# Kernel tuning notes

Measured on AMD Instinct MI355X. Metric: run time of the kernel, lower is better.

## Reference

```python
import jax, jax.numpy as jnp
import numpy as np

N = 100_000          # nodes
E = 1_600_000        # random edges (self-loops added inside gat_conv, as PyG does)
F_IN = 14
DIM = 8
HEADS = 8
NEG_SLOPE = 0.2      # PyG GATConv default negative_slope


def _gat_conv(x, edge_index, W, a_src, a_dst, bias, heads, dim, concat):
    """Faithful PyG GATConv (eval mode): self-loops, per-head linear,
    leaky-relu attention logits, segment softmax over dst, scatter-add."""
    n = x.shape[0]
    loop = jnp.arange(n)
    src = jnp.concatenate([edge_index[0], loop])   # source j
    dst = jnp.concatenate([edge_index[1], loop])   # target i (aggregation index)

    h = (x @ W).reshape(n, heads, dim)             # [N, H, D]
    alpha_src = jnp.einsum('nhd,hd->nh', h, a_src)  # [N, H]
    alpha_dst = jnp.einsum('nhd,hd->nh', h, a_dst)

    e = jax.nn.leaky_relu(alpha_src[src] + alpha_dst[dst], NEG_SLOPE)  # [E', H]
    # segment softmax over incoming edges of each dst node
    m = jax.ops.segment_max(e, dst, num_segments=n)                     # [N, H]
    ex = jnp.exp(e - m[dst])
    s = jax.ops.segment_sum(ex, dst, num_segments=n)
    alpha = ex / (s[dst] + 1e-16)                                       # [E', H]

    msg = h[src] * alpha[:, :, None]                                    # [E', H, D]
    out = jax.ops.segment_sum(msg, dst, num_segments=n)                 # [N, H, D]
    out = out.reshape(n, heads * dim) if concat else out.mean(axis=1)
    return out + bias


def setup_inputs() -> dict:
    key = jax.random.key(0)
    ks = jax.random.split(key, 10)
    x = jax.random.normal(ks[0], (N, F_IN), jnp.float32)
    edge_index = jax.random.randint(ks[1], (2, E), 0, N, dtype=jnp.int64)
    W1 = jax.random.normal(ks[2], (F_IN, HEADS * DIM), jnp.float32) * 0.3
    att_src1 = jax.random.normal(ks[3], (HEADS, DIM), jnp.float32) * 0.3
    att_dst1 = jax.random.normal(ks[4], (HEADS, DIM), jnp.float32) * 0.3
    bias1 = jnp.zeros((HEADS * DIM,), jnp.float32)
    W2 = jax.random.normal(ks[5], (HEADS * DIM, DIM), jnp.float32) * 0.15
    att_src2 = jax.random.normal(ks[6], (1, DIM), jnp.float32) * 0.3
    att_dst2 = jax.random.normal(ks[7], (1, DIM), jnp.float32) * 0.3
    bias2 = jnp.zeros((DIM,), jnp.float32)
    return {"x": x, "edge_index": edge_index,
            "W1": W1, "att_src1": att_src1, "att_dst1": att_dst1, "bias1": bias1,
            "W2": W2, "att_src2": att_src2, "att_dst2": att_dst2, "bias2": bias2}


def reference(x, edge_index, W1, att_src1, att_dst1, bias1,
              W2, att_src2, att_dst2, bias2):
    # dropout layers are identity in eval mode
    h = jax.nn.elu(_gat_conv(x, edge_index, W1, att_src1, att_dst1, bias1,
                             HEADS, DIM, concat=True))      # [N, 64]
    out = _gat_conv(h, edge_index, W2, att_src2, att_dst2, bias2,
                    1, DIM, concat=False)                   # [N, 8]
    return out
```

## Files before the change

### kernel.cpp

```cpp
#include <hip/hip_runtime.h>
#include <math.h>

#define F_IN 14
#define NSLOPE 0.2f
#define BSHIFT 7
#define BSZ 128
#define CAP 4096
#define NBMAX 1024
#define NCHUNKMAX 256
#define CHUNK 8192

typedef __attribute__((ext_vector_type(8))) unsigned short u16x8;

__device__ __forceinline__ float leaky(float v) { return v >= 0.f ? v : NSLOPE * v; }

__device__ __forceinline__ float b2f(unsigned short u) {
    union { float f; unsigned int i; } v; v.i = ((unsigned int)u) << 16; return v.f;
}
__device__ __forceinline__ unsigned short f2b(float f) {
    union { float f; unsigned int i; } v; v.f = f;
    unsigned int r = v.i + 0x7FFFu + ((v.i >> 16) & 1u);
    return (unsigned short)(r >> 16);
}

__device__ __forceinline__ int wave_incl_scan(int x) {
#pragma unroll
    for (int off = 1; off < 64; off <<= 1) {
        int v = __shfl_up(x, off, 64);
        if ((threadIdx.x & 63) >= off) x += v;
    }
    return x;
}


__global__ __launch_bounds__(1024)
void k_scatter_k1(const int* __restrict__ ei, int E,
                  int* __restrict__ stage, int* __restrict__ tab, int NB,
                  int nchunk,
                  const float* __restrict__ x,
                  const float* __restrict__ W1,
                  const float* __restrict__ a_src,
                  const float* __restrict__ a_dst,
                  unsigned short* __restrict__ h1b,
                  unsigned short* __restrict__ as1b,
                  float* __restrict__ ad1,
                  int N)
{
    __shared__ int hist[NBMAX];
    __shared__ int cur[NBMAX];
    __shared__ int srt[CHUNK];
    __shared__ int wsum[16];
    __shared__ float W[F_IN * 64];
    int t = threadIdx.x;
    if (blockIdx.x < (unsigned)nchunk) {
        int base = blockIdx.x * CHUNK;
        int end = min(base + CHUNK, E);
        int cnt = end - base;
        hist[t] = 0;
        __syncthreads();
        for (int k = base + t; k < end; k += 1024)
            atomicAdd(&hist[ei[E + k] >> BSHIFT], 1);
        __syncthreads();
        int hx = hist[t];
        int incl = wave_incl_scan(hx);
        int wid = t >> 6;
        if ((t & 63) == 63) wsum[wid] = incl;
        __syncthreads();
        int wpre = 0;
#pragma unroll
        for (int w = 0; w < 15; ++w) wpre += (w < wid) ? wsum[w] : 0;
        int exb = incl - hx + wpre;
        cur[t] = exb;
        if (t < NB) tab[(size_t)blockIdx.x * (NBMAX + 1) + t] = exb;
        if (t == 0) tab[(size_t)blockIdx.x * (NBMAX + 1) + NB] = cnt;
        __syncthreads();
        for (int k = base + t; k < end; k += 1024) {
            int j = ei[k];
            int i = ei[E + k];
            int key = i >> BSHIFT;
            int pos = atomicAdd(&cur[key], 1);
            srt[pos] = j | ((i & (BSZ - 1)) << 17);
        }
        __syncthreads();
        int cnt4 = cnt & ~3;
        for (int k = t * 4; k < cnt4; k += 4096) {
            int4 v = *(const int4*)&srt[k];
            *(int4*)&stage[base + k] = v;
        }
        if (t < (cnt & 3)) stage[base + cnt4 + t] = srt[cnt4 + t];
    } else {
        for (int idx = t; idx < F_IN * 64; idx += 1024) W[idx] = W1[idx];
        __syncthreads();
        int node = (blockIdx.x - nchunk) * 16 + (t >> 6);
        int f = t & 63;
        if (node >= N) return;
        const float* xr = x + (size_t)node * F_IN;
        float h = 0.f;
#pragma unroll
        for (int k = 0; k < F_IN; ++k) h += xr[k] * W[k * 64 + f];
        int head = f >> 3, d = f & 7;
        float vs = h * a_src[head * 8 + d];
        float vd = h * a_dst[head * 8 + d];
        vs += __shfl_xor(vs, 1, 8); vs += __shfl_xor(vs, 2, 8); vs += __shfl_xor(vs, 4, 8);
        vd += __shfl_xor(vd, 1, 8); vd += __shfl_xor(vd, 2, 8); vd += __shfl_xor(vd, 4, 8);
        if (d == 0) {
            as1b[node * 8 + head] = f2b(vs);
            ad1[node * 8 + head] = vd;
        }
        h1b[(size_t)node * 64 + f] = f2b(h);
    }
}


__global__ __launch_bounds__(256)
void pass2(const int* __restrict__ stage, const int* __restrict__ tab, int nchunk,
           int* __restrict__ rowstart, int* __restrict__ deg,
           int* __restrict__ csr, int N) {
    int b = blockIdx.x;
    int node0 = b << BSHIFT;
    int nn = min(BSZ, N - node0);
    int base = b * CAP;
    __shared__ int segstart[NCHUNKMAX];
    __shared__ int cum[NCHUNKMAX];
    __shared__ int hist[BSZ];
    __shared__ int cur[BSZ];
    __shared__ int wsum[4];
    __shared__ int wsum2[2];
    __shared__ int recs[CAP];
    int t = threadIdx.x;
    int len = 0, s = 0;
    if (t < nchunk) {
        const int* tr = tab + (size_t)t * (NBMAX + 1);
        s = tr[b];
        len = tr[b + 1] - s;
    }
    segstart[t] = s;
    if (t < BSZ) hist[t] = 0;
    int incl = wave_incl_scan(len);
    int wid = t >> 6;
    if ((t & 63) == 63) wsum[wid] = incl;
    __syncthreads();
    int wpre = 0;
#pragma unroll
    for (int w = 0; w < 3; ++w) wpre += (w < wid) ? wsum[w] : 0;
    cum[t] = incl + wpre;
    __syncthreads();
    int cnt = min(cum[NCHUNKMAX - 1], CAP);
    for (int k = t; k < cnt; k += 256) {
        int lo = 0, hi = NCHUNKMAX - 1;
        while (lo < hi) {
            int mid = (lo + hi) >> 1;
            if (cum[mid] > k) hi = mid; else lo = mid + 1;
        }
        int prev = lo ? cum[lo - 1] : 0;
        int r = stage[lo * CHUNK + segstart[lo] + (k - prev)];
        recs[k] = r;
        atomicAdd(&hist[r >> 17], 1);
    }
    __syncthreads();
    int hx = (t < BSZ) ? hist[t] : 0;
    int incl2 = wave_incl_scan(hx);
    if (t < BSZ && (t & 63) == 63) wsum2[t >> 6] = incl2;
    __syncthreads();
    if (t < nn) {
        int ex = incl2 - hx + ((t >= 64) ? wsum2[0] : 0);
        rowstart[node0 + t] = base + ex;
        deg[node0 + t] = hist[t];
        cur[t] = base + ex;
    }
    __syncthreads();
    for (int k = t; k < cnt; k += 256) {
        int r = recs[k];
        int pos = atomicAdd(&cur[r >> 17], 1);
        csr[pos] = r & 0x1FFFF;
    }
}


__global__ void k2_fused(const int* __restrict__ rowstart,
                         const int* __restrict__ deg,
                         const int* __restrict__ csr,
                         const unsigned short* __restrict__ h1b,
                         const unsigned short* __restrict__ as1b,
                         const float* __restrict__ ad1,
                         const float* __restrict__ bias1,
                         const float* __restrict__ W2,
                         const float* __restrict__ asw2,
                         const float* __restrict__ adw2,
                         float* __restrict__ h2,
                         float* __restrict__ as2,
                         float* __restrict__ ad2, int N)
{
    int t = threadIdx.x;
    int node = blockIdx.x * 32 + (t >> 3);
    int head = t & 7;
    if (node >= N) return;
    float adi = ad1[node * 8 + head];
    float asi = b2f(as1b[node * 8 + head]);
    float ex = __expf(leaky(asi + adi));
    float den = ex;
    u16x8 a = *(const u16x8*)(h1b + (size_t)node * 64 + head * 8);
    float n[8];
#pragma unroll
    for (int u = 0; u < 8; ++u) n[u] = ex * b2f(a[u]);
    int base = rowstart[node], cnt = deg[node];
    int k = 0;
    for (; k + 4 <= cnt; k += 4) {
        int j0 = csr[base + k];
        int j1 = csr[base + k + 1];
        int j2 = csr[base + k + 2];
        int j3 = csr[base + k + 3];
        float e0 = __expf(leaky(b2f(as1b[j0 * 8 + head]) + adi));
        float e1 = __expf(leaky(b2f(as1b[j1 * 8 + head]) + adi));
        float e2 = __expf(leaky(b2f(as1b[j2 * 8 + head]) + adi));
        float e3 = __expf(leaky(b2f(as1b[j3 * 8 + head]) + adi));
        u16x8 r0 = *(const u16x8*)(h1b + (size_t)j0 * 64 + head * 8);
        u16x8 r1 = *(const u16x8*)(h1b + (size_t)j1 * 64 + head * 8);
        u16x8 r2 = *(const u16x8*)(h1b + (size_t)j2 * 64 + head * 8);
        u16x8 r3 = *(const u16x8*)(h1b + (size_t)j3 * 64 + head * 8);
        den += (e0 + e1) + (e2 + e3);
#pragma unroll
        for (int u = 0; u < 8; ++u)
            n[u] += (e0 * b2f(r0[u]) + e1 * b2f(r1[u])) + (e2 * b2f(r2[u]) + e3 * b2f(r3[u]));
    }
    for (; k < cnt; ++k) {
        int j0 = csr[base + k];
        float e0 = __expf(leaky(b2f(as1b[j0 * 8 + head]) + adi));
        u16x8 r0 = *(const u16x8*)(h1b + (size_t)j0 * 64 + head * 8);
        den += e0;
#pragma unroll
        for (int u = 0; u < 8; ++u) n[u] += e0 * b2f(r0[u]);
    }
    float inv = 1.f / (den + 1e-16f);
    float v[8];
    const float* bp = bias1 + head * 8;
#pragma unroll
    for (int u = 0; u < 8; ++u) {
        float w = n[u] * inv + bp[u];
        v[u] = w > 0.f ? w : (__expf(w) - 1.f);
    }
    float p[8];
    const float* wrow = W2 + head * 64;
#pragma unroll
    for (int o = 0; o < 8; ++o) {
        float s = 0.f;
#pragma unroll
        for (int u = 0; u < 8; ++u) s += v[u] * wrow[u * 8 + o];
        p[o] = s;
    }
#pragma unroll
    for (int o = 0; o < 8; ++o) {
        p[o] += __shfl_xor(p[o], 1, 8);
        p[o] += __shfl_xor(p[o], 2, 8);
        p[o] += __shfl_xor(p[o], 4, 8);
    }
    float vs = 0.f, vd = 0.f;
#pragma unroll
    for (int o = 0; o < 8; ++o) { vs += p[o] * asw2[o]; vd += p[o] * adw2[o]; }
    if (head == 0) { as2[node] = vs; ad2[node] = vd; }
    float hv = p[0];
#pragma unroll
    for (int o = 1; o < 8; ++o) hv = (head == o) ? p[o] : hv;
    h2[(size_t)node * 8 + head] = hv;
}


__global__ void k4_gather_l2(const int* __restrict__ rowstart,
                             const int* __restrict__ deg,
                             const int* __restrict__ csr,
                             const float* __restrict__ h2,
                             const float* __restrict__ as2,
                             const float* __restrict__ ad2,
                             const float* __restrict__ bias2,
                             float* __restrict__ out, int N)
{
    int t = threadIdx.x;
    int node = blockIdx.x * 32 + (t >> 3);
    int d = t & 7;
    if (node >= N) return;
    float adi = ad2[node];
    float ex = __expf(leaky(as2[node] + adi));
    float den = ex;
    float num = ex * h2[(size_t)node * 8 + d];
    int base = rowstart[node], cnt = deg[node];
    int k = 0;
    for (; k + 8 <= cnt; k += 8) {
        int j0 = csr[base + k];
        int j1 = csr[base + k + 1];
        int j2 = csr[base + k + 2];
        int j3 = csr[base + k + 3];
        int j4 = csr[base + k + 4];
        int j5 = csr[base + k + 5];
        int j6 = csr[base + k + 6];
        int j7 = csr[base + k + 7];
        float e0 = __expf(leaky(as2[j0] + adi));
        float e1 = __expf(leaky(as2[j1] + adi));
        float e2 = __expf(leaky(as2[j2] + adi));
        float e3 = __expf(leaky(as2[j3] + adi));
        float e4 = __expf(leaky(as2[j4] + adi));
        float e5 = __expf(leaky(as2[j5] + adi));
        float e6 = __expf(leaky(as2[j6] + adi));
        float e7 = __expf(leaky(as2[j7] + adi));
        float v0 = h2[(size_t)j0 * 8 + d];
        float v1 = h2[(size_t)j1 * 8 + d];
        float v2 = h2[(size_t)j2 * 8 + d];
        float v3 = h2[(size_t)j3 * 8 + d];
        float v4 = h2[(size_t)j4 * 8 + d];
        float v5 = h2[(size_t)j5 * 8 + d];
        float v6 = h2[(size_t)j6 * 8 + d];
        float v7 = h2[(size_t)j7 * 8 + d];
        den += ((e0 + e1) + (e2 + e3)) + ((e4 + e5) + (e6 + e7));
        num += ((e0 * v0 + e1 * v1) + (e2 * v2 + e3 * v3))
             + ((e4 * v4 + e5 * v5) + (e6 * v6 + e7 * v7));
    }
    for (; k + 4 <= cnt; k += 4) {
        int j0 = csr[base + k];
        int j1 = csr[base + k + 1];
        int j2 = csr[base + k + 2];
        int j3 = csr[base + k + 3];
        float e0 = __expf(leaky(as2[j0] + adi));
        float e1 = __expf(leaky(as2[j1] + adi));
        float e2 = __expf(leaky(as2[j2] + adi));
        float e3 = __expf(leaky(as2[j3] + adi));
        float v0 = h2[(size_t)j0 * 8 + d];
        float v1 = h2[(size_t)j1 * 8 + d];
        float v2 = h2[(size_t)j2 * 8 + d];
        float v3 = h2[(size_t)j3 * 8 + d];
        den += (e0 + e1) + (e2 + e3);
        num += (e0 * v0 + e1 * v1) + (e2 * v2 + e3 * v3);
    }
    for (; k < cnt; ++k) {
        int j0 = csr[base + k];
        float e0 = __expf(leaky(as2[j0] + adi));
        den += e0;
        num += e0 * h2[(size_t)j0 * 8 + d];
    }
    out[(size_t)node * 8 + d] = num / (den + 1e-16f) + bias2[d];
}


extern "C" void kernel_launch(void* const* d_in, const int* in_sizes, int n_in,
                              void* d_out, int out_size, void* d_ws, size_t ws_size,
                              hipStream_t stream) {
    const float* x    = (const float*)d_in[0];
    const int*   ei   = (const int*)d_in[1];
    const float* W1   = (const float*)d_in[2];
    const float* asw1 = (const float*)d_in[3];
    const float* adw1 = (const float*)d_in[4];
    const float* b1   = (const float*)d_in[5];
    const float* W2   = (const float*)d_in[6];
    const float* asw2 = (const float*)d_in[7];
    const float* adw2 = (const float*)d_in[8];
    const float* b2   = (const float*)d_in[9];
    float* out = (float*)d_out;

    int N = in_sizes[0] / F_IN;
    int E = in_sizes[1] / 2;
    int NB = (N + BSZ - 1) >> BSHIFT;
    int nchunk = (E + CHUNK - 1) / CHUNK;
    int k1blk = (N + 15) / 16;

    float* fw  = (float*)d_ws;
    float* h2  = fw;
    float* as2 = h2  + (size_t)N * 8;
    float* ad2 = as2 + (size_t)N;
    float* ad1 = ad2 + (size_t)N;
    unsigned short* h1b  = (unsigned short*)(ad1 + (size_t)N * 8);
    unsigned short* as1b = h1b + (size_t)N * 64;
    int* deg      = (int*)(as1b + (size_t)N * 8);
    int* rowstart = deg + N;
    int* csr      = rowstart + N;
    int* stage    = csr + (size_t)NB * CAP;
    int* tab      = stage + (size_t)nchunk * CHUNK;

    k_scatter_k1<<<nchunk + k1blk, 1024, 0, stream>>>(ei, E, stage, tab, NB, nchunk,
                                                      x, W1, asw1, adw1, h1b, as1b, ad1, N);
    pass2<<<NB, 256, 0, stream>>>(stage, tab, nchunk, rowstart, deg, csr, N);

    k2_fused<<<(N + 31) / 32, 256, 0, stream>>>(rowstart, deg, csr, h1b, as1b, ad1,
                                                b1, W2, asw2, adw2, h2, as2, ad2, N);

    k4_gather_l2<<<(N + 31) / 32, 256, 0, stream>>>(rowstart, deg, csr, h2, as2, ad2, b2, out, N);
}
```

Baseline: 124.9 us.

## Recompute attention logits from gathered features instead of storing per-node arrays

```diff
diff --git a/kernel.cpp b/kernel.cpp
--- a/kernel.cpp
+++ b/kernel.cpp
@@ -39,11 +39,7 @@
                   int nchunk,
                   const float* __restrict__ x,
                   const float* __restrict__ W1,
-                  const float* __restrict__ a_src,
-                  const float* __restrict__ a_dst,
                   unsigned short* __restrict__ h1b,
-                  unsigned short* __restrict__ as1b,
-                  float* __restrict__ ad1,
                   int N)
 {
     __shared__ int hist[NBMAX];
@@ -98,15 +94,6 @@
         float h = 0.f;
 #pragma unroll
         for (int k = 0; k < F_IN; ++k) h += xr[k] * W[k * 64 + f];
-        int head = f >> 3, d = f & 7;
-        float vs = h * a_src[head * 8 + d];
-        float vd = h * a_dst[head * 8 + d];
-        vs += __shfl_xor(vs, 1, 8); vs += __shfl_xor(vs, 2, 8); vs += __shfl_xor(vs, 4, 8);
-        vd += __shfl_xor(vd, 1, 8); vd += __shfl_xor(vd, 2, 8); vd += __shfl_xor(vd, 4, 8);
-        if (d == 0) {
-            as1b[node * 8 + head] = f2b(vs);
-            ad1[node * 8 + head] = vd;
-        }
         h1b[(size_t)node * 64 + f] = f2b(h);
     }
 }
@@ -181,28 +168,34 @@
                          const int* __restrict__ deg,
                          const int* __restrict__ csr,
                          const unsigned short* __restrict__ h1b,
-                         const unsigned short* __restrict__ as1b,
-                         const float* __restrict__ ad1,
+                         const float* __restrict__ asw1,
+                         const float* __restrict__ adw1,
                          const float* __restrict__ bias1,
                          const float* __restrict__ W2,
-                         const float* __restrict__ asw2,
-                         const float* __restrict__ adw2,
-                         float* __restrict__ h2,
-                         float* __restrict__ as2,
-                         float* __restrict__ ad2, int N)
+                         float* __restrict__ h2, int N)
 {
     int t = threadIdx.x;
     int node = blockIdx.x * 32 + (t >> 3);
     int head = t & 7;
     if (node >= N) return;
-    float adi = ad1[node * 8 + head];
-    float asi = b2f(as1b[node * 8 + head]);
+    float4 w0 = *(const float4*)(asw1 + head * 8);
+    float4 w1 = *(const float4*)(asw1 + head * 8 + 4);
+    float aw[8] = { w0.x, w0.y, w0.z, w0.w, w1.x, w1.y, w1.z, w1.w };
+    float4 d0 = *(const float4*)(adw1 + head * 8);
+    float4 d1 = *(const float4*)(adw1 + head * 8 + 4);
+    u16x8 a = *(const u16x8*)(h1b + (size_t)node * 64 + head * 8);
+    float av[8];
+#pragma unroll
+    for (int u = 0; u < 8; ++u) av[u] = b2f(a[u]);
+    float asi = av[0]*aw[0]+av[1]*aw[1]+av[2]*aw[2]+av[3]*aw[3]
+              + av[4]*aw[4]+av[5]*aw[5]+av[6]*aw[6]+av[7]*aw[7];
+    float adi = av[0]*d0.x+av[1]*d0.y+av[2]*d0.z+av[3]*d0.w
+              + av[4]*d1.x+av[5]*d1.y+av[6]*d1.z+av[7]*d1.w;
     float ex = __expf(leaky(asi + adi));
     float den = ex;
-    u16x8 a = *(const u16x8*)(h1b + (size_t)node * 64 + head * 8);
     float n[8];
 #pragma unroll
-    for (int u = 0; u < 8; ++u) n[u] = ex * b2f(a[u]);
+    for (int u = 0; u < 8; ++u) n[u] = ex * av[u];
     int base = rowstart[node], cnt = deg[node];
     int k = 0;
     for (; k + 4 <= cnt; k += 4) {
@@ -210,26 +203,44 @@
         int j1 = csr[base + k + 1];
         int j2 = csr[base + k + 2];
         int j3 = csr[base + k + 3];
-        float e0 = __expf(leaky(b2f(as1b[j0 * 8 + head]) + adi));
-        float e1 = __expf(leaky(b2f(as1b[j1 * 8 + head]) + adi));
-        float e2 = __expf(leaky(b2f(as1b[j2 * 8 + head]) + adi));
-        float e3 = __expf(leaky(b2f(as1b[j3 * 8 + head]) + adi));
         u16x8 r0 = *(const u16x8*)(h1b + (size_t)j0 * 64 + head * 8);
         u16x8 r1 = *(const u16x8*)(h1b + (size_t)j1 * 64 + head * 8);
         u16x8 r2 = *(const u16x8*)(h1b + (size_t)j2 * 64 + head * 8);
         u16x8 r3 = *(const u16x8*)(h1b + (size_t)j3 * 64 + head * 8);
+        float f0[8], f1[8], f2[8], f3[8];
+#pragma unroll
+        for (int u = 0; u < 8; ++u) {
+            f0[u] = b2f(r0[u]); f1[u] = b2f(r1[u]);
+            f2[u] = b2f(r2[u]); f3[u] = b2f(r3[u]);
+        }
+        float s0 = 0.f, s1 = 0.f, s2 = 0.f, s3 = 0.f;
+#pragma unroll
+        for (int u = 0; u < 8; ++u) {
+            s0 += f0[u] * aw[u]; s1 += f1[u] * aw[u];
+            s2 += f2[u] * aw[u]; s3 += f3[u] * aw[u];
+        }
+        float e0 = __expf(leaky(s0 + adi));
+        float e1 = __expf(leaky(s1 + adi));
+        float e2 = __expf(leaky(s2 + adi));
+        float e3 = __expf(leaky(s3 + adi));
         den += (e0 + e1) + (e2 + e3);
 #pragma unroll
         for (int u = 0; u < 8; ++u)
-            n[u] += (e0 * b2f(r0[u]) + e1 * b2f(r1[u])) + (e2 * b2f(r2[u]) + e3 * b2f(r3[u]));
+            n[u] += (e0 * f0[u] + e1 * f1[u]) + (e2 * f2[u] + e3 * f3[u]);
     }
     for (; k < cnt; ++k) {
         int j0 = csr[base + k];
-        float e0 = __expf(leaky(b2f(as1b[j0 * 8 + head]) + adi));
         u16x8 r0 = *(const u16x8*)(h1b + (size_t)j0 * 64 + head * 8);
+        float f0[8];
+#pragma unroll
+        for (int u = 0; u < 8; ++u) f0[u] = b2f(r0[u]);
+        float s0 = 0.f;
+#pragma unroll
+        for (int u = 0; u < 8; ++u) s0 += f0[u] * aw[u];
+        float e0 = __expf(leaky(s0 + adi));
         den += e0;
 #pragma unroll
-        for (int u = 0; u < 8; ++u) n[u] += e0 * b2f(r0[u]);
+        for (int u = 0; u < 8; ++u) n[u] += e0 * f0[u];
     }
     float inv = 1.f / (den + 1e-16f);
     float v[8];
@@ -254,10 +265,6 @@
         p[o] += __shfl_xor(p[o], 2, 8);
         p[o] += __shfl_xor(p[o], 4, 8);
     }
-    float vs = 0.f, vd = 0.f;
-#pragma unroll
-    for (int o = 0; o < 8; ++o) { vs += p[o] * asw2[o]; vd += p[o] * adw2[o]; }
-    if (head == 0) { as2[node] = vs; ad2[node] = vd; }
     float hv = p[0];
 #pragma unroll
     for (int o = 1; o < 8; ++o) hv = (head == o) ? p[o] : hv;
@@ -269,8 +276,8 @@
                              const int* __restrict__ deg,
                              const int* __restrict__ csr,
                              const float* __restrict__ h2,
-                             const float* __restrict__ as2,
-                             const float* __restrict__ ad2,
+                             const float* __restrict__ asw2,
+                             const float* __restrict__ adw2,
                              const float* __restrict__ bias2,
                              float* __restrict__ out, int N)
 {
@@ -278,62 +285,49 @@
     int node = blockIdx.x * 32 + (t >> 3);
     int d = t & 7;
     if (node >= N) return;
-    float adi = ad2[node];
-    float ex = __expf(leaky(as2[node] + adi));
+    float aswd = asw2[d], adwd = adw2[d];
+    float selfv = h2[(size_t)node * 8 + d];
+    float td = selfv * adwd;
+    td += __shfl_xor(td, 1, 8); td += __shfl_xor(td, 2, 8); td += __shfl_xor(td, 4, 8);
+    float adi = td;
+    float ts = selfv * aswd;
+    ts += __shfl_xor(ts, 1, 8); ts += __shfl_xor(ts, 2, 8); ts += __shfl_xor(ts, 4, 8);
+    float ex = __expf(leaky(ts + adi));
     float den = ex;
-    float num = ex * h2[(size_t)node * 8 + d];
+    float num = ex * selfv;
     int base = rowstart[node], cnt = deg[node];
     int k = 0;
-    for (; k + 8 <= cnt; k += 8) {
-        int j0 = csr[base + k];
-        int j1 = csr[base + k + 1];
-        int j2 = csr[base + k + 2];
-        int j3 = csr[base + k + 3];
-        int j4 = csr[base + k + 4];
-        int j5 = csr[base + k + 5];
-        int j6 = csr[base + k + 6];
-        int j7 = csr[base + k + 7];
-        float e0 = __expf(leaky(as2[j0] + adi));
-        float e1 = __expf(leaky(as2[j1] + adi));
-        float e2 = __expf(leaky(as2[j2] + adi));
-        float e3 = __expf(leaky(as2[j3] + adi));
-        float e4 = __expf(leaky(as2[j4] + adi));
-        float e5 = __expf(leaky(as2[j5] + adi));
-        float e6 = __expf(leaky(as2[j6] + adi));
-        float e7 = __expf(leaky(as2[j7] + adi));
-        float v0 = h2[(size_t)j0 * 8 + d];
-        float v1 = h2[(size_t)j1 * 8 + d];
-        float v2 = h2[(size_t)j2 * 8 + d];
-        float v3 = h2[(size_t)j3 * 8 + d];
-        float v4 = h2[(size_t)j4 * 8 + d];
-        float v5 = h2[(size_t)j5 * 8 + d];
-        float v6 = h2[(size_t)j6 * 8 + d];
-        float v7 = h2[(size_t)j7 * 8 + d];
-        den += ((e0 + e1) + (e2 + e3)) + ((e4 + e5) + (e6 + e7));
-        num += ((e0 * v0 + e1 * v1) + (e2 * v2 + e3 * v3))
-             + ((e4 * v4 + e5 * v5) + (e6 * v6 + e7 * v7));
-    }
     for (; k + 4 <= cnt; k += 4) {
         int j0 = csr[base + k];
         int j1 = csr[base + k + 1];
         int j2 = csr[base + k + 2];
         int j3 = csr[base + k + 3];
-        float e0 = __expf(leaky(as2[j0] + adi));
-        float e1 = __expf(leaky(as2[j1] + adi));
-        float e2 = __expf(leaky(as2[j2] + adi));
-        float e3 = __expf(leaky(as2[j3] + adi));
         float v0 = h2[(size_t)j0 * 8 + d];
         float v1 = h2[(size_t)j1 * 8 + d];
         float v2 = h2[(size_t)j2 * 8 + d];
         float v3 = h2[(size_t)j3 * 8 + d];
+        float t0 = v0 * aswd, t1 = v1 * aswd, t2 = v2 * aswd, t3 = v3 * aswd;
+        t0 += __shfl_xor(t0, 1, 8); t1 += __shfl_xor(t1, 1, 8);
+        t2 += __shfl_xor(t2, 1, 8); t3 += __shfl_xor(t3, 1, 8);
+        t0 += __shfl_xor(t0, 2, 8); t1 += __shfl_xor(t1, 2, 8);
+        t2 += __shfl_xor(t2, 2, 8); t3 += __shfl_xor(t3, 2, 8);
+        t0 += __shfl_xor(t0, 4, 8); t1 += __shfl_xor(t1, 4, 8);
+        t2 += __shfl_xor(t2, 4, 8); t3 += __shfl_xor(t3, 4, 8);
+        float e0 = __expf(leaky(t0 + adi));
+        float e1 = __expf(leaky(t1 + adi));
+        float e2 = __expf(leaky(t2 + adi));
+        float e3 = __expf(leaky(t3 + adi));
         den += (e0 + e1) + (e2 + e3);
         num += (e0 * v0 + e1 * v1) + (e2 * v2 + e3 * v3);
     }
     for (; k < cnt; ++k) {
         int j0 = csr[base + k];
-        float e0 = __expf(leaky(as2[j0] + adi));
+        float v0 = h2[(size_t)j0 * 8 + d];
+        float t0 = v0 * aswd;
+        t0 += __shfl_xor(t0, 1, 8); t0 += __shfl_xor(t0, 2, 8); t0 += __shfl_xor(t0, 4, 8);
+        float e0 = __expf(leaky(t0 + adi));
         den += e0;
-        num += e0 * h2[(size_t)j0 * 8 + d];
+        num += e0 * v0;
     }
     out[(size_t)node * 8 + d] = num / (den + 1e-16f) + bias2[d];
 }
@@ -362,23 +356,20 @@
 
     float* fw  = (float*)d_ws;
     float* h2  = fw;
-    float* as2 = h2  + (size_t)N * 8;
-    float* ad2 = as2 + (size_t)N;
-    float* ad1 = ad2 + (size_t)N;
-    unsigned short* h1b  = (unsigned short*)(ad1 + (size_t)N * 8);
-    unsigned short* as1b = h1b + (size_t)N * 64;
-    int* deg      = (int*)(as1b + (size_t)N * 8);
+    unsigned short* h1b = (unsigned short*)(h2 + (size_t)N * 8);
+    int* deg      = (int*)(h1b + (size_t)N * 64);
     int* rowstart = deg + N;
     int* csr      = rowstart + N;
     int* stage    = csr + (size_t)NB * CAP;
     int* tab      = stage + (size_t)nchunk * CHUNK;
 
     k_scatter_k1<<<nchunk + k1blk, 1024, 0, stream>>>(ei, E, stage, tab, NB, nchunk,
-                                                      x, W1, asw1, adw1, h1b, as1b, ad1, N);
+                                                      x, W1, h1b, N);
     pass2<<<NB, 256, 0, stream>>>(stage, tab, nchunk, rowstart, deg, csr, N);
 
-    k2_fused<<<(N + 31) / 32, 256, 0, stream>>>(rowstart, deg, csr, h1b, as1b, ad1,
-                                                b1, W2, asw2, adw2, h2, as2, ad2, N);
-
-    k4_gather_l2<<<(N + 31) / 32, 256, 0, stream>>>(rowstart, deg, csr, h2, as2, ad2, b2, out, N);
-}
+    k2_fused<<<(N + 31) / 32, 256, 0, stream>>>(rowstart, deg, csr, h1b,
+                                                asw1, adw1, b1, W2, h2, N);
+
+    k4_gather_l2<<<(N + 31) / 32, 256, 0, stream>>>(rowstart, deg, csr, h2,
+                                                    asw2, adw2, b2, out, N);
+}
```

New measurement: 122.3 us. 1.02x faster.
